# Optimization experiments

Measured on AMD Instinct MI355X. Metric: run time of the kernel, lower is better.

Reference implementation:

```python
import math
import jax, jax.numpy as jnp
import numpy as np

DIM = 1024
N_HEADS = 16
HEAD_DIM = DIM // N_HEADS
SEQ_LEN = 2048
BASE = 10000.0
EPS = 1e-5


def rope_cache(seq_len, dim):
    pos = jnp.arange(seq_len, dtype=jnp.float32)[:, None]          # (S,1)
    di = jnp.arange(0, dim, 2, dtype=jnp.float32) / dim            # (d/2,)
    theta = pos * jnp.exp(-di * math.log(BASE))                    # (S,d/2)
    cos = jnp.repeat(jnp.cos(theta), 2, axis=1)                    # (S,d)
    sin = jnp.repeat(jnp.sin(theta), 2, axis=1)
    return cos, sin


def rotate_half(x):
    # NOTE: faithful to source: concatenate (-odd, even), not interleave
    x1 = x[..., ::2]
    x2 = x[..., 1::2]
    return jnp.concatenate((-x2, x1), axis=-1)


def layernorm(x, gamma, beta):
    mu = jnp.mean(x, axis=-1, keepdims=True)
    var = jnp.var(x, axis=-1, keepdims=True)
    return (x - mu) * jax.lax.rsqrt(var + EPS) * gamma + beta


def setup_inputs() -> dict:
    key = jax.random.key(0)
    ks = jax.random.split(key, 7)
    s = 1.0 / math.sqrt(DIM)
    return {
        "x": jax.random.normal(ks[0], (2, SEQ_LEN, DIM), dtype=jnp.float32),
        "Wq": jax.random.normal(ks[1], (DIM, DIM), dtype=jnp.float32) * s,
        "Wk": jax.random.normal(ks[2], (DIM, DIM), dtype=jnp.float32) * s,
        "Wv": jax.random.normal(ks[3], (DIM, DIM), dtype=jnp.float32) * s,
        "q_gamma": jnp.ones((HEAD_DIM,), jnp.float32),
        "q_beta": jnp.zeros((HEAD_DIM,), jnp.float32),
        "k_gamma": jnp.ones((HEAD_DIM,), jnp.float32),
        "k_beta": jnp.zeros((HEAD_DIM,), jnp.float32),
        "Wo": jax.random.normal(ks[4], (DIM, DIM), dtype=jnp.float32) * s,
        "bo": jnp.zeros((DIM,), jnp.float32),
    }


def reference(x, Wq, Wk, Wv, q_gamma, q_beta, k_gamma, k_beta, Wo, bo):
    B, S, D = x.shape
    H, hd = N_HEADS, HEAD_DIM
    # QKV projections (torch Linear: x @ W.T)
    q = (x @ Wq.T).reshape(B, S, H, hd).transpose(0, 2, 1, 3)  # (B,H,S,hd)
    k = (x @ Wk.T).reshape(B, S, H, hd).transpose(0, 2, 1, 3)
    v = (x @ Wv.T).reshape(B, S, H, hd).transpose(0, 2, 1, 3)
    # QK-norm over head_dim
    q = layernorm(q, q_gamma, q_beta)
    k = layernorm(k, k_gamma, k_beta)
    # RoPE
    cos, sin = rope_cache(S, hd)  # (S,hd)
    cos = cos[None, None]
    sin = sin[None, None]
    q = q * cos + rotate_half(q) * sin
    k = k * cos + rotate_half(k) * sin
    # causal attention
    scale = 1.0 / math.sqrt(hd)
    scores = scale * jnp.einsum('bhqd,bhkd->bhqk', q, k)
    mask = jnp.tril(jnp.ones((S, S), dtype=bool))
    scores = jnp.where(mask, scores, -jnp.inf)
    attn = jax.nn.softmax(scores, axis=-1)
    out = jnp.einsum('bhqk,bhkd->bhqd', attn, v)
    out = out.transpose(0, 2, 1, 3).reshape(B, S, D)
    return out @ Wo.T + bo
```

## Files before the change

### kernel.cpp

```cpp
#include <hip/hip_runtime.h>
#include <hip/hip_bf16.h>

#define SEQ   2048
#define NH    16
#define HD    64
#define BATCH 2
#define DIMM  1024

typedef __attribute__((ext_vector_type(8))) __bf16 bfrag;
typedef __attribute__((ext_vector_type(4))) float f32x4;

__device__ __forceinline__ short f2b(float f) {
  unsigned x = __float_as_uint(f);
  x += 0x7fff + ((x >> 16) & 1);
  return (short)(x >> 16);
}
__device__ __forceinline__ float b2f(short s) {
  unsigned u = ((unsigned)(unsigned short)s) << 16;
  return __uint_as_float(u);
}
__device__ __forceinline__ short f2b_pk(float f) {
  unsigned r;
  asm("v_cvt_pk_bf16_f32 %0, %1, %1" : "=v"(r) : "v"(f));
  return (short)r;
}

__device__ __forceinline__ void gload16(const void* g, void* l) {
  __builtin_amdgcn_global_load_lds(
      (const __attribute__((address_space(1))) void*)g,
      (__attribute__((address_space(3))) void*)l, 16, 0, 0);
}

__global__ __launch_bounds__(256) void k_prep(
    const float* __restrict__ x, const float* __restrict__ w0,
    const float* __restrict__ w1, const float* __restrict__ w2,
    const float* __restrict__ w3, short* __restrict__ xb,
    short* __restrict__ wb, float* __restrict__ cstab) {
  int b = blockIdx.x;
  if (b < 4096) {
    int i = b * 256 + threadIdx.x;
    float4 v = reinterpret_cast<const float4*>(x)[i];
    short4 o;
    o.x = f2b(v.x); o.y = f2b(v.y); o.z = f2b(v.z); o.w = f2b(v.w);
    reinterpret_cast<short4*>(xb)[i] = o;
  } else if (b < 8192) {
    int bb = b - 4096;
    int widx = bb >> 10;
    const float* src = widx == 0 ? w0 : (widx == 1 ? w1 : (widx == 2 ? w2 : w3));
    int i = (bb & 1023) * 256 + threadIdx.x;
    float4 v = reinterpret_cast<const float4*>(src)[i];
    short4 o;
    o.x = f2b(v.x); o.y = f2b(v.y); o.z = f2b(v.z); o.w = f2b(v.w);
    reinterpret_cast<short4*>(wb + (size_t)widx * 1048576)[i] = o;
  } else {
    int gid = (b - 8192) * 256 + threadIdx.x;
    int s = gid >> 5, i = gid & 31;
    float freq = expf(-(float)(2 * i) * (1.0f / 64.0f) * 9.210340371976184f);
    float th = (float)s * freq;
    cstab[gid * 2]     = cosf(th);
    cstab[gid * 2 + 1] = sinf(th);
  }
}

__global__ __launch_bounds__(256) void k_gemm_qkv(
    const short* __restrict__ xb, const short* __restrict__ wb,
    short* __restrict__ Qh, short* __restrict__ Kh, short* __restrict__ Vt) {
  __shared__ alignas(16) short As[2][128 * 64];
  __shared__ alignas(16) short Bs[2][128 * 64];
  const int tid = threadIdx.x;
  const int lane = tid & 63, w = tid >> 6;
  const int wr = w >> 1, wc = w & 1;
  const int id = blockIdx.x;
  const int xcd = id & 7, j = id >> 3;
  const int bn = xcd * 3 + j % 3;
  const int bm = j / 3;
  const int widx = bn >> 3;
  const int brow0 = (bn & 7) * 128;
  const short* Wp = wb + (size_t)widx * (1 << 20);

  const int l15 = lane & 15, lq = lane >> 4, l7 = lane & 7;
  const int srow = lane >> 3;
  const int sslot = l7 ^ srow;

  f32x4 acc[4][4] = {};

  auto STAGE = [&](int buf, int kk) {
#pragma unroll
    for (int p = 0; p < 4; ++p) {
      int rr = p * 32 + w * 8 + srow;
      gload16(&xb[(size_t)(bm * 128 + rr) * 1024 + kk + sslot * 8],
              &As[buf][p * 2048 + w * 512]);
      gload16(&Wp[(size_t)(brow0 + rr) * 1024 + kk + sslot * 8],
              &Bs[buf][p * 2048 + w * 512]);
    }
  };

  STAGE(0, 0);
  __syncthreads();
  int cur = 0;
#pragma unroll 1
  for (int t = 0; t < 16; ++t) {
    if (t + 1 < 16) STAGE(cur ^ 1, (t + 1) * 64);
#pragma unroll
    for (int ks = 0; ks < 2; ++ks) {
      bfrag af[4], bf[4];
      int slot = (ks * 4 + lq) ^ l7;
#pragma unroll
      for (int mi = 0; mi < 4; ++mi)
        af[mi] = *(const bfrag*)&As[cur][(wr * 64 + mi * 16 + l15) * 64 + slot * 8];
#pragma unroll
      for (int ni = 0; ni < 4; ++ni)
        bf[ni] = *(const bfrag*)&Bs[cur][(wc * 64 + ni * 16 + l15) * 64 + slot * 8];
      __builtin_amdgcn_s_setprio(1);
#pragma unroll
      for (int mi = 0; mi < 4; ++mi)
#pragma unroll
        for (int ni = 0; ni < 4; ++ni)
          acc[mi][ni] = __builtin_amdgcn_mfma_f32_16x16x32_bf16(af[mi], bf[ni], acc[mi][ni], 0, 0, 0);
      __builtin_amdgcn_s_setprio(0);
    }
    __syncthreads();
    cur ^= 1;
  }

  if (widx < 2) {
    short* dst = widx == 0 ? Qh : Kh;
#pragma unroll
    for (int mi = 0; mi < 4; ++mi) {
#pragma unroll
      for (int ni = 0; ni < 4; ++ni) {
        int ng = bn * 128 + wc * 64 + ni * 16 + l15;
        int col = ng & 1023, h = col >> 6, d = col & 63;
#pragma unroll
        for (int r = 0; r < 4; ++r) {
          int mg = bm * 128 + wr * 64 + mi * 16 + lq * 4 + r;
          int b = mg >> 11, s = mg & 2047;
          dst[((size_t)((b * 16 + h) * 2048 + s)) * 64 + d] = f2b(acc[mi][ni][r]);
        }
      }
    }
  } else {
#pragma unroll
    for (int mi = 0; mi < 4; ++mi) {
#pragma unroll
      for (int ni = 0; ni < 4; ++ni) {
        int ng = bn * 128 + wc * 64 + ni * 16 + l15;
        int col = ng & 1023, h = col >> 6, d = col & 63;
        int mg0 = bm * 128 + wr * 64 + mi * 16 + lq * 4;
        int b = mg0 >> 11, s0 = mg0 & 2047;
        short4 sv;
        sv.x = f2b(acc[mi][ni][0]); sv.y = f2b(acc[mi][ni][1]);
        sv.z = f2b(acc[mi][ni][2]); sv.w = f2b(acc[mi][ni][3]);
        *reinterpret_cast<short4*>(
            &Vt[((size_t)((b * 16 + h) * 64 + d)) * 2048 + s0]) = sv;
      }
    }
  }
}

__global__ __launch_bounds__(256) void k_ln_rope(
    short* __restrict__ Qh, short* __restrict__ Kh,
    const float* __restrict__ qg, const float* __restrict__ qb_,
    const float* __restrict__ kg, const float* __restrict__ kb_,
    const float* __restrict__ cstab) {
  __shared__ float Ysh[32 * 64];
  const int tid = threadIdx.x;
  const int rloc = tid >> 3;
  const int g = tid & 7;
  const int d0 = g * 8;
  const int row = blockIdx.x * 32 + rloc;
  const int which = blockIdx.y;
  short* ptr = which ? Kh : Qh;
  const float* gamma = which ? kg : qg;
  const float* beta  = which ? kb_ : qb_;
  const float alpha = which ? 1.0f : 0.18033688011112042f;
  const int s = row & 2047;

  short vs[8];
  *reinterpret_cast<uint4*>(vs) =
      *reinterpret_cast<const uint4*>(&ptr[(size_t)row * 64 + d0]);
  float x[8];
#pragma unroll
  for (int j = 0; j < 8; ++j) x[j] = b2f(vs[j]);
  float s1 = 0.0f, s2 = 0.0f;
#pragma unroll
  for (int j = 0; j < 8; ++j) { s1 += x[j]; s2 = fmaf(x[j], x[j], s2); }
#pragma unroll
  for (int off = 1; off < 8; off <<= 1) {
    s1 += __shfl_xor(s1, off, 8);
    s2 += __shfl_xor(s2, off, 8);
  }
  float mu = s1 * (1.0f / 64.0f);
  float var = s2 * (1.0f / 64.0f) - mu * mu;
  float rs = rsqrtf(var + 1e-5f);

  float gv[8], bv[8];
  *reinterpret_cast<float4*>(&gv[0]) = *reinterpret_cast<const float4*>(&gamma[d0]);
  *reinterpret_cast<float4*>(&gv[4]) = *reinterpret_cast<const float4*>(&gamma[d0 + 4]);
  *reinterpret_cast<float4*>(&bv[0]) = *reinterpret_cast<const float4*>(&beta[d0]);
  *reinterpret_cast<float4*>(&bv[4]) = *reinterpret_cast<const float4*>(&beta[d0 + 4]);
  float y[8];
#pragma unroll
  for (int j = 0; j < 8; ++j)
    y[j] = ((x[j] - mu) * rs * gv[j] + bv[j]) * alpha;

  *reinterpret_cast<float4*>(&Ysh[rloc * 64 + d0])     = *reinterpret_cast<float4*>(&y[0]);
  *reinterpret_cast<float4*>(&Ysh[rloc * 64 + d0 + 4]) = *reinterpret_cast<float4*>(&y[4]);
  __syncthreads();

  float2 cs4[4];
  *reinterpret_cast<float4*>(&cs4[0]) =
      *reinterpret_cast<const float4*>(&cstab[((size_t)s * 32 + g * 4) * 2]);
  *reinterpret_cast<float4*>(&cs4[2]) =
      *reinterpret_cast<const float4*>(&cstab[((size_t)s * 32 + g * 4 + 2) * 2]);

  short o[8];
#pragma unroll
  for (int j = 0; j < 8; ++j) {
    int d = d0 + j;
    float pv = (d < 32) ? Ysh[rloc * 64 + 2 * d + 1]
                        : Ysh[rloc * 64 + 2 * (d - 32)];
    float c = cs4[j >> 1].x, sn = cs4[j >> 1].y;
    float ov = (d < 32) ? (y[j] * c - pv * sn) : (y[j] * c + pv * sn);
    o[j] = f2b_pk(ov);
  }
  *reinterpret_cast<uint4*>(&ptr[(size_t)row * 64 + d0]) =
      *reinterpret_cast<uint4*>(o);
}

__global__ __launch_bounds__(256) void k_attn(
    const short* __restrict__ Qh, const short* __restrict__ Kh,
    const short* __restrict__ Vtg, short* __restrict__ Ob) {
  __shared__ alignas(16) short Ks[2][64 * 64];
  __shared__ alignas(16) short Vs[2][64 * 64];
  __shared__ alignas(16) short Ps[4][16 * 64];
  const int id = blockIdx.x;
  const int xcd = id & 7;
  const int idx = id >> 3;
  const int qt = 31 - (idx >> 2);
  const int bh = xcd * 4 + (idx & 3);
  const int b = bh >> 4, h = bh & 15;
  const int tid = threadIdx.x, lane = tid & 63, w = tid >> 6;
  const short* Qp = Qh + (size_t)bh * SEQ * 64;
  const short* Kp = Kh + (size_t)bh * SEQ * 64;
  const short* Vp = Vtg + (size_t)bh * 64 * SEQ;

  const int srow = lane >> 3;
  const int sslot = (lane & 7) ^ srow;

  const int l15 = lane & 15;
  const int l7 = lane & 7;
  const int lq = lane >> 4;

  auto STAGE = [&](int buf, int kb) {
#pragma unroll
    for (int j = 0; j < 2; ++j) {
      int rr = w * 16 + j * 8 + srow;
      gload16(&Kp[(size_t)(kb * 64 + rr) * 64 + sslot * 8],
              &Ks[buf][w * 1024 + j * 512]);
      gload16(&Vp[(size_t)rr * 2048 + kb * 64 + sslot * 8],
              &Vs[buf][w * 1024 + j * 512]);
    }
  };

  const int nkb = qt + 1;

  const int qrow_l = qt * 64 + w * 16 + l15;
  bfrag qf[2];
#pragma unroll
  for (int c = 0; c < 2; ++c)
    qf[c] = *(const bfrag*)&Qp[(size_t)qrow_l * 64 + c * 32 + lq * 8];

  f32x4 oacc[4] = {};
  float lrow[4] = {0.0f, 0.0f, 0.0f, 0.0f};

  auto body = [&](int kb, int cur, bool diag) {
    f32x4 sacc[4] = {};
    __builtin_amdgcn_s_setprio(1);
#pragma unroll
    for (int c2 = 0; c2 < 4; ++c2) {
      int krow = c2 * 16 + l15;
#pragma unroll
      for (int dc = 0; dc < 2; ++dc) {
        int slot = (dc * 4 + lq) ^ l7;
        bfrag kf = *(const bfrag*)&Ks[cur][krow * 64 + slot * 8];
        sacc[c2] = __builtin_amdgcn_mfma_f32_16x16x32_bf16(qf[dc], kf, sacc[c2], 0, 0, 0);
      }
    }
    __builtin_amdgcn_s_setprio(0);

    const int qg0 = qt * 64 + w * 16 + lq * 4;
#pragma unroll
    for (int r = 0; r < 4; ++r) {
      float pv4[4];
#pragma unroll
      for (int c2 = 0; c2 < 4; ++c2) {
        float s2 = sacc[c2][r];
        if (diag && (kb * 64 + c2 * 16 + l15 > qg0 + r)) s2 = -1e30f;
        pv4[c2] = __builtin_amdgcn_exp2f(s2);
      }
      lrow[r] += (pv4[0] + pv4[1]) + (pv4[2] + pv4[3]);
      int row = lq * 4 + r;
#pragma unroll
      for (int c2 = 0; c2 < 4; ++c2) {
        int swz = (c2 * 2 + (l15 >> 3)) ^ (row & 7);
        Ps[w][row * 64 + swz * 8 + (l15 & 7)] = f2b_pk(pv4[c2]);
      }
    }

    bfrag pf[2];
#pragma unroll
    for (int kf2 = 0; kf2 < 2; ++kf2)
      pf[kf2] = *(const bfrag*)&Ps[w][l15 * 64 + (((kf2 * 4 + lq) ^ l7) * 8)];
    __builtin_amdgcn_s_setprio(1);
#pragma unroll
    for (int dc = 0; dc < 4; ++dc) {
      int drow = dc * 16 + l15;
#pragma unroll
      for (int kf2 = 0; kf2 < 2; ++kf2) {
        int slot = (kf2 * 4 + lq) ^ l7;
        bfrag vf = *(const bfrag*)&Vs[cur][drow * 64 + slot * 8];
        oacc[dc] = __builtin_amdgcn_mfma_f32_16x16x32_bf16(pf[kf2], vf, oacc[dc], 0, 0, 0);
      }
    }
    __builtin_amdgcn_s_setprio(0);
  };

  STAGE(0, 0);
  __syncthreads();

  int cur = 0;
#pragma unroll 1
  for (int kb = 0; kb < nkb - 1; ++kb) {
    STAGE(cur ^ 1, kb + 1);
    body(kb, cur, false);
    __syncthreads();
    cur ^= 1;
  }
  body(nkb - 1, cur, true);

  float inv[4];
#pragma unroll
  for (int r = 0; r < 4; ++r) {
#pragma unroll
    for (int off = 1; off < 16; off <<= 1) lrow[r] += __shfl_xor(lrow[r], off);
    inv[r] = 1.0f / lrow[r];
  }
#pragma unroll
  for (int dc = 0; dc < 4; ++dc) {
#pragma unroll
    for (int r = 0; r < 4; ++r) {
      int qg = qt * 64 + w * 16 + lq * 4 + r;
      Ob[(size_t)(b * SEQ + qg) * 1024 + h * 64 + dc * 16 + l15] =
          f2b(oacc[dc][r] * inv[r]);
    }
  }
}

__global__ __launch_bounds__(256) void k_gemm_out(
    const short* __restrict__ Ab, const short* __restrict__ Wp,
    const float* __restrict__ bo, float* __restrict__ out) {
  __shared__ alignas(16) short As[2][64 * 64];
  __shared__ alignas(16) short Bs[2][128 * 64];
  const int tid = threadIdx.x;
  const int lane = tid & 63, w = tid >> 6;
  const int id = blockIdx.x;
  const int bn = id & 7, bm = id >> 3;
  const int brow0 = bn * 128;

  const int l15 = lane & 15, lq = lane >> 4, l7 = lane & 7;
  const int srow = lane >> 3;
  const int sslot = l7 ^ srow;

  f32x4 acc[4][2] = {};

  auto STAGE = [&](int buf, int kk) {
#pragma unroll
    for (int p = 0; p < 2; ++p) {
      int rr = p * 32 + w * 8 + srow;
      gload16(&Ab[(size_t)(bm * 64 + rr) * 1024 + kk + sslot * 8],
              &As[buf][p * 2048 + w * 512]);
    }
#pragma unroll
    for (int p = 0; p < 4; ++p) {
      int rr = p * 32 + w * 8 + srow;
      gload16(&Wp[(size_t)(brow0 + rr) * 1024 + kk + sslot * 8],
              &Bs[buf][p * 2048 + w * 512]);
    }
  };

  STAGE(0, 0);
  __syncthreads();
  int cur = 0;
#pragma unroll 1
  for (int t = 0; t < 16; ++t) {
    if (t + 1 < 16) STAGE(cur ^ 1, (t + 1) * 64);
#pragma unroll
    for (int ks = 0; ks < 2; ++ks) {
      bfrag af[4], bf[2];
      int slot = (ks * 4 + lq) ^ l7;
#pragma unroll
      for (int mi = 0; mi < 4; ++mi)
        af[mi] = *(const bfrag*)&As[cur][(mi * 16 + l15) * 64 + slot * 8];
#pragma unroll
      for (int ni = 0; ni < 2; ++ni)
        bf[ni] = *(const bfrag*)&Bs[cur][(w * 32 + ni * 16 + l15) * 64 + slot * 8];
      __builtin_amdgcn_s_setprio(1);
#pragma unroll
      for (int mi = 0; mi < 4; ++mi)
#pragma unroll
        for (int ni = 0; ni < 2; ++ni)
          acc[mi][ni] = __builtin_amdgcn_mfma_f32_16x16x32_bf16(af[mi], bf[ni], acc[mi][ni], 0, 0, 0);
      __builtin_amdgcn_s_setprio(0);
    }
    __syncthreads();
    cur ^= 1;
  }

#pragma unroll
  for (int mi = 0; mi < 4; ++mi) {
#pragma unroll
    for (int ni = 0; ni < 2; ++ni) {
      int ng = bn * 128 + w * 32 + ni * 16 + l15;
      float bias = bo[ng];
#pragma unroll
      for (int r = 0; r < 4; ++r) {
        int mg = bm * 64 + mi * 16 + lq * 4 + r;
        out[(size_t)mg * 1024 + ng] = acc[mi][ni][r] + bias;
      }
    }
  }
}

extern "C" void kernel_launch(void* const* d_in, const int* in_sizes, int n_in,
                              void* d_out, int out_size, void* d_ws, size_t ws_size,
                              hipStream_t stream) {
  const float* x  = (const float*)d_in[0];
  const float* Wq = (const float*)d_in[1];
  const float* Wk = (const float*)d_in[2];
  const float* Wv = (const float*)d_in[3];
  const float* qgamma = (const float*)d_in[4];
  const float* qbeta  = (const float*)d_in[5];
  const float* kgamma = (const float*)d_in[6];
  const float* kbeta  = (const float*)d_in[7];
  const float* Wo = (const float*)d_in[8];
  const float* bo = (const float*)d_in[9];
  float* out = (float*)d_out;

  char* ws = (char*)d_ws;
  short* xb    = (short*)(ws);
  short* wb    = (short*)(ws + 8388608);
  short* Qh    = (short*)(ws + 16777216);
  short* Kh    = (short*)(ws + 25165824);
  short* Vt    = (short*)(ws + 33554432);
  short* Obuf  = (short*)(ws + 41943040);
  float* cstab = (float*)(ws + 50331648);

  k_prep<<<8448, 256, 0, stream>>>(x, Wq, Wk, Wv, Wo, xb, wb, cstab);

  k_gemm_qkv<<<768, 256, 0, stream>>>(xb, wb, Qh, Kh, Vt);
  k_ln_rope<<<dim3(2048, 2), 256, 0, stream>>>(
      Qh, Kh, qgamma, qbeta, kgamma, kbeta, cstab);
  k_attn<<<1024, 256, 0, stream>>>(Qh, Kh, Vt, Obuf);
  k_gemm_out<<<512, 256, 0, stream>>>(Obuf, wb + 3145728, bo, out);
}
```

Measured before the change: 117.5 us.

## Split attention tile 2x2 across waves to reuse K/V fragments across query subtiles

The attention kernel's wave layout changes from four waves each owning 16 query rows over all 64 keys to a 2x2 grid. Each wave now computes 32 query rows against 32 keys for QK^T and 32 query rows by 32 head dims for PV. Each K and V fragment loaded from shared memory now feeds two MFMAs, which halves LDS reads per MFMA. The cost is a shared P tile with a block-wide barrier in every iteration, plus a cross-wave reduction of row sums through shared memory at the end.

```diff
diff --git a/kernel.cpp b/kernel.cpp
--- a/kernel.cpp
+++ b/kernel.cpp
@@ -233,7 +233,7 @@
     const short* __restrict__ Vtg, short* __restrict__ Ob) {
   __shared__ alignas(16) short Ks[2][64 * 64];
   __shared__ alignas(16) short Vs[2][64 * 64];
-  __shared__ alignas(16) short Ps[4][16 * 64];
+  __shared__ alignas(16) short Ps[64 * 64];
   const int id = blockIdx.x;
   const int xcd = id & 7;
   const int idx = id >> 3;
@@ -241,6 +241,7 @@
   const int bh = xcd * 4 + (idx & 3);
   const int b = bh >> 4, h = bh & 15;
   const int tid = threadIdx.x, lane = tid & 63, w = tid >> 6;
+  const int wq = w >> 1, wk = w & 1;
   const short* Qp = Qh + (size_t)bh * SEQ * 64;
   const short* Kp = Kh + (size_t)bh * SEQ * 64;
   const short* Vp = Vtg + (size_t)bh * 64 * SEQ;
@@ -265,62 +266,76 @@
 
   const int nkb = qt + 1;
 
-  const int qrow_l = qt * 64 + w * 16 + l15;
-  bfrag qf[2];
-#pragma unroll
-  for (int c = 0; c < 2; ++c)
-    qf[c] = *(const bfrag*)&Qp[(size_t)qrow_l * 64 + c * 32 + lq * 8];
-
-  f32x4 oacc[4] = {};
-  float lrow[4] = {0.0f, 0.0f, 0.0f, 0.0f};
+  bfrag qf[2][2];
+#pragma unroll
+  for (int qt2 = 0; qt2 < 2; ++qt2)
+#pragma unroll
+    for (int dc = 0; dc < 2; ++dc)
+      qf[qt2][dc] = *(const bfrag*)&Qp[
+          (size_t)(qt * 64 + wq * 32 + qt2 * 16 + l15) * 64 + dc * 32 + lq * 8];
+
+  f32x4 oacc[2][2] = {};
+  float lrow[2][4] = {};
 
   auto body = [&](int kb, int cur, bool diag) {
-    f32x4 sacc[4] = {};
+    f32x4 sacc[2][2] = {};
     __builtin_amdgcn_s_setprio(1);
 #pragma unroll
-    for (int c2 = 0; c2 < 4; ++c2) {
-      int krow = c2 * 16 + l15;
+    for (int kt = 0; kt < 2; ++kt) {
+      int krow = wk * 32 + kt * 16 + l15;
 #pragma unroll
       for (int dc = 0; dc < 2; ++dc) {
-        int slot = (dc * 4 + lq) ^ l7;
-        bfrag kf = *(const bfrag*)&Ks[cur][krow * 64 + slot * 8];
-        sacc[c2] = __builtin_amdgcn_mfma_f32_16x16x32_bf16(qf[dc], kf, sacc[c2], 0, 0, 0);
+        bfrag kf = *(const bfrag*)&Ks[cur][krow * 64 + ((dc * 4 + lq) ^ l7) * 8];
+#pragma unroll
+        for (int qt2 = 0; qt2 < 2; ++qt2)
+          sacc[qt2][kt] = __builtin_amdgcn_mfma_f32_16x16x32_bf16(
+              qf[qt2][dc], kf, sacc[qt2][kt], 0, 0, 0);
       }
     }
     __builtin_amdgcn_s_setprio(0);
 
-    const int qg0 = qt * 64 + w * 16 + lq * 4;
-#pragma unroll
-    for (int r = 0; r < 4; ++r) {
-      float pv4[4];
-#pragma unroll
-      for (int c2 = 0; c2 < 4; ++c2) {
-        float s2 = sacc[c2][r];
-        if (diag && (kb * 64 + c2 * 16 + l15 > qg0 + r)) s2 = -1e30f;
-        pv4[c2] = __builtin_amdgcn_exp2f(s2);
-      }
-      lrow[r] += (pv4[0] + pv4[1]) + (pv4[2] + pv4[3]);
-      int row = lq * 4 + r;
-#pragma unroll
-      for (int c2 = 0; c2 < 4; ++c2) {
-        int swz = (c2 * 2 + (l15 >> 3)) ^ (row & 7);
-        Ps[w][row * 64 + swz * 8 + (l15 & 7)] = f2b_pk(pv4[c2]);
-      }
-    }
-
-    bfrag pf[2];
-#pragma unroll
-    for (int kf2 = 0; kf2 < 2; ++kf2)
-      pf[kf2] = *(const bfrag*)&Ps[w][l15 * 64 + (((kf2 * 4 + lq) ^ l7) * 8)];
+    const int qg0 = qt * 64 + wq * 32 + lq * 4;
+#pragma unroll
+    for (int qt2 = 0; qt2 < 2; ++qt2) {
+#pragma unroll
+      for (int kt = 0; kt < 2; ++kt) {
+        int kcol = wk * 32 + kt * 16 + l15;
+        int kglob = kb * 64 + kcol;
+#pragma unroll
+        for (int r = 0; r < 4; ++r) {
+          float s2 = sacc[qt2][kt][r];
+          if (diag && (kglob > qg0 + qt2 * 16 + r)) s2 = -1e30f;
+          float p = __builtin_amdgcn_exp2f(s2);
+          lrow[qt2][r] += p;
+          int qrow = wq * 32 + qt2 * 16 + lq * 4 + r;
+          int swz = (kcol >> 3) ^ (qrow & 7);
+          Ps[qrow * 64 + swz * 8 + (kcol & 7)] = f2b_pk(p);
+        }
+      }
+    }
+
+    asm volatile("s_waitcnt lgkmcnt(0)" ::: "memory");
+    __builtin_amdgcn_s_barrier();
+    __builtin_amdgcn_sched_barrier(0);
+
+    bfrag pa[2][2];
+#pragma unroll
+    for (int qt2 = 0; qt2 < 2; ++qt2)
+#pragma unroll
+      for (int kc = 0; kc < 2; ++kc)
+        pa[qt2][kc] = *(const bfrag*)&Ps[
+            (wq * 32 + qt2 * 16 + l15) * 64 + ((kc * 4 + lq) ^ l7) * 8];
     __builtin_amdgcn_s_setprio(1);
 #pragma unroll
-    for (int dc = 0; dc < 4; ++dc) {
-      int drow = dc * 16 + l15;
-#pragma unroll
-      for (int kf2 = 0; kf2 < 2; ++kf2) {
-        int slot = (kf2 * 4 + lq) ^ l7;
-        bfrag vf = *(const bfrag*)&Vs[cur][drow * 64 + slot * 8];
-        oacc[dc] = __builtin_amdgcn_mfma_f32_16x16x32_bf16(pf[kf2], vf, oacc[dc], 0, 0, 0);
+    for (int dt = 0; dt < 2; ++dt) {
+      int drow = wk * 32 + dt * 16 + l15;
+#pragma unroll
+      for (int kc = 0; kc < 2; ++kc) {
+        bfrag vf = *(const bfrag*)&Vs[cur][drow * 64 + ((kc * 4 + lq) ^ l7) * 8];
+#pragma unroll
+        for (int qt2 = 0; qt2 < 2; ++qt2)
+          oacc[qt2][dt] = __builtin_amdgcn_mfma_f32_16x16x32_bf16(
+              pa[qt2][kc], vf, oacc[qt2][dt], 0, 0, 0);
       }
     }
     __builtin_amdgcn_s_setprio(0);
@@ -339,20 +354,45 @@
   }
   body(nkb - 1, cur, true);
 
-  float inv[4];
-#pragma unroll
-  for (int r = 0; r < 4; ++r) {
-#pragma unroll
-    for (int off = 1; off < 16; off <<= 1) lrow[r] += __shfl_xor(lrow[r], off);
-    inv[r] = 1.0f / lrow[r];
-  }
-#pragma unroll
-  for (int dc = 0; dc < 4; ++dc) {
+#pragma unroll
+  for (int qt2 = 0; qt2 < 2; ++qt2)
 #pragma unroll
     for (int r = 0; r < 4; ++r) {
-      int qg = qt * 64 + w * 16 + lq * 4 + r;
-      Ob[(size_t)(b * SEQ + qg) * 1024 + h * 64 + dc * 16 + l15] =
-          f2b(oacc[dc][r] * inv[r]);
+#pragma unroll
+      for (int off = 1; off < 16; off <<= 1)
+        lrow[qt2][r] += __shfl_xor(lrow[qt2][r], off);
+    }
+  __syncthreads();
+  float* Lf = (float*)Ps;
+  if (l15 == 0) {
+#pragma unroll
+    for (int qt2 = 0; qt2 < 2; ++qt2)
+#pragma unroll
+      for (int r = 0; r < 4; ++r)
+        Lf[(wq * 2 + wk) * 32 + qt2 * 16 + lq * 4 + r] = lrow[qt2][r];
+  }
+  __syncthreads();
+  float inv[2][4];
+#pragma unroll
+  for (int qt2 = 0; qt2 < 2; ++qt2)
+#pragma unroll
+    for (int r = 0; r < 4; ++r) {
+      int idx2 = qt2 * 16 + lq * 4 + r;
+      inv[qt2][r] = 1.0f / (Lf[(wq * 2 + 0) * 32 + idx2] +
+                            Lf[(wq * 2 + 1) * 32 + idx2]);
+    }
+
+#pragma unroll
+  for (int qt2 = 0; qt2 < 2; ++qt2) {
+#pragma unroll
+    for (int dt = 0; dt < 2; ++dt) {
+#pragma unroll
+      for (int r = 0; r < 4; ++r) {
+        int qg = qt * 64 + wq * 32 + qt2 * 16 + lq * 4 + r;
+        int d = wk * 32 + dt * 16 + l15;
+        Ob[(size_t)(b * SEQ + qg) * 1024 + h * 64 + d] =
+            f2b(oacc[qt2][dt][r] * inv[qt2][r]);
+      }
     }
   }
 }
```

Result: no change. 115.9 us (-1.3%).
